# Kernel tuning notes

Hardware: AMD Instinct MI355X
Metric: run time of the kernel (lower is better)

The kernel has to match this reference:

```python
import jax, jax.numpy as jnp
import numpy as np

C = 256
RED = 2
CR = C // RED
B, D, H, W = 1, 16, 32, 32


def setup_inputs() -> dict:
    key = jax.random.key(0)
    ks = jax.random.split(key, 9)
    def w(k, o, i):
        return jax.random.normal(k, (o, i), dtype=jnp.float32) * (2.0 / i) ** 0.5
    return {
        "x": jax.random.normal(ks[0], (B, C, D, H, W), dtype=jnp.float32),
        "Wq": w(ks[1], CR, C), "bq": jnp.zeros((CR,), jnp.float32),
        "Wk": w(ks[2], CR, C), "bk": jnp.zeros((CR,), jnp.float32),
        "Wv": w(ks[3], CR, C), "bv": jnp.zeros((CR,), jnp.float32),
        "Wo": w(ks[4], C, CR) * 0.02, "bo": jnp.zeros((C,), jnp.float32),
    }


def reference(x, Wq, bq, Wk, bk, Wv, bv, Wo, bo):
    b, c, d, h, w = x.shape
    n = d * h * w
    scale = 1.0 / (c ** 0.5)
    xf = x.reshape(b, c, n)                      # [B, C, N]
    # 1x1x1 convs == per-voxel channel GEMMs
    q = jnp.einsum('oc,bcn->bno', Wq, xf) + bq   # [B, N, Cr]
    k = jnp.einsum('oc,bcn->bon', Wk, xf) + bk[:, None]  # [B, Cr, N]
    v = jnp.einsum('oc,bcn->bno', Wv, xf) + bv   # [B, N, Cr]
    attn = jnp.einsum('bnc,bcm->bnm', q, k) * scale      # [B, N, N]
    attn = jax.nn.softmax(attn, axis=-1)
    o = jnp.einsum('bnm,bmc->bnc', attn, v)      # [B, N, Cr]
    out = jnp.einsum('oc,bnc->bon', Wo, o) + bo[:, None]  # [B, C, N]
    return x + out.reshape(b, c, d, h, w)
```

## Files before the change

kernel.cpp:

```cpp
#include <hip/hip_runtime.h>

#define NTOK 16384
#define CCH  256
#define DH   128
#define KSPLIT 4

typedef float f32x4  __attribute__((ext_vector_type(4)));
typedef short bf16x8 __attribute__((ext_vector_type(8)));
typedef short bf16x4 __attribute__((ext_vector_type(4)));

__device__ __forceinline__ unsigned short f2bf(float f) {
    unsigned int u = __builtin_bit_cast(unsigned int, f);
    u += 0x7fffu + ((u >> 16) & 1u);
    return (unsigned short)(u >> 16);
}
__device__ __forceinline__ float bf2f(unsigned short h) {
    unsigned int u = ((unsigned int)h) << 16;
    return __builtin_bit_cast(float, u);
}
__device__ __forceinline__ unsigned short f2bf_fast(float f) {
    unsigned int u = __builtin_bit_cast(unsigned int, f);
    return (unsigned short)((u + 0x8000u) >> 16);
}
__device__ __forceinline__ void load_lds16(const unsigned short* g, unsigned short* l) {
    __builtin_amdgcn_global_load_lds(
        (const __attribute__((address_space(1))) unsigned int*)g,
        (__attribute__((address_space(3))) unsigned int*)l, 16, 0, 0);
}

__global__ __launch_bounds__(256) void prep_w(
    const float* __restrict__ Wq, const float* __restrict__ Wk,
    const float* __restrict__ Wv, const float* __restrict__ Wo,
    unsigned short* __restrict__ Wqkv_bf, unsigned short* __restrict__ Wo_bf)
{
    int idx4 = (blockIdx.x * 256 + threadIdx.x) * 4;
    if (idx4 < 98304) {
        int wch = idx4 >> 15;
        int off = idx4 & 32767;
        const float* W = (wch == 0) ? Wq : ((wch == 1) ? Wk : Wv);
        float4 v = *(const float4*)(W + off);
        bf16x4 pk = { (short)f2bf(v.x), (short)f2bf(v.y),
                      (short)f2bf(v.z), (short)f2bf(v.w) };
        *(bf16x4*)(Wqkv_bf + idx4) = pk;
    } else {
        int off = idx4 - 98304;
        float4 v = *(const float4*)(Wo + off);
        bf16x4 pk = { (short)f2bf(v.x), (short)f2bf(v.y),
                      (short)f2bf(v.z), (short)f2bf(v.w) };
        *(bf16x4*)(Wo_bf + off) = pk;
    }
}

__global__ __launch_bounds__(256) void qkv_fused(
    const float* __restrict__ x, const unsigned short* __restrict__ Wqkv_bf,
    const float* __restrict__ bq, const float* __restrict__ bk,
    const float* __restrict__ bv,
    unsigned short* __restrict__ Qb, unsigned short* __restrict__ Kb,
    unsigned short* __restrict__ Vb)
{
    __shared__ unsigned short lX[32 * 264];
    __shared__ unsigned short lW[3 * DH * 40];

    const int t    = threadIdx.x;
    const int wave = t >> 6, lane = t & 63, l16 = lane & 15, quad = lane >> 4;
    const int nt   = blockIdx.x;

#pragma unroll
    for (int pass = 0; pass < 8; ++pass) {
        int c  = pass * 32 + (t >> 3);
        int n4 = t & 7;
        float4 xv = *(const float4*)(x + c * NTOK + nt * 32 + n4 * 4);
        lX[(n4 * 4 + 0) * 264 + c] = f2bf(xv.x);
        lX[(n4 * 4 + 1) * 264 + c] = f2bf(xv.y);
        lX[(n4 * 4 + 2) * 264 + c] = f2bf(xv.z);
        lX[(n4 * 4 + 3) * 264 + c] = f2bf(xv.w);
    }

    f32x4 acc[3][2][2];
#pragma unroll
    for (int wch = 0; wch < 3; ++wch)
#pragma unroll
        for (int os = 0; os < 2; ++os)
#pragma unroll
            for (int ns = 0; ns < 2; ++ns) acc[wch][os][ns] = (f32x4){0, 0, 0, 0};

    for (int kc8 = 0; kc8 < 8; ++kc8) {
        __syncthreads();
#pragma unroll
        for (int wch = 0; wch < 3; ++wch) {
            const unsigned short* Wb = Wqkv_bf + wch * 32768;
#pragma unroll
            for (int p = 0; p < 2; ++p) {
                int s = p * 256 + t;
                int row = s >> 2, oct = s & 3;
                bf16x8 wv = *(const bf16x8*)(Wb + row * CCH + kc8 * 32 + oct * 8);
                *(bf16x8*)(&lW[wch * DH * 40 + row * 40 + oct * 8]) = wv;
            }
        }
        __syncthreads();

        bf16x8 bfr[2];
#pragma unroll
        for (int ns = 0; ns < 2; ++ns)
            bfr[ns] = *(const bf16x8*)(&lX[(ns * 16 + l16) * 264 + kc8 * 32 + quad * 8]);
#pragma unroll
        for (int wch = 0; wch < 3; ++wch)
#pragma unroll
            for (int os = 0; os < 2; ++os) {
                bf16x8 afr = *(const bf16x8*)(&lW[wch * DH * 40 + (wave * 32 + os * 16 + l16) * 40 + quad * 8]);
                acc[wch][os][0] = __builtin_amdgcn_mfma_f32_16x16x32_bf16(afr, bfr[0], acc[wch][os][0], 0, 0, 0);
                acc[wch][os][1] = __builtin_amdgcn_mfma_f32_16x16x32_bf16(afr, bfr[1], acc[wch][os][1], 0, 0, 0);
            }
    }

    unsigned short* lE = lX;

#pragma unroll
    for (int wch = 0; wch < 2; ++wch) {
        const float* bias = (wch == 0) ? bq : bk;
        const float oscale = (wch == 0) ? 0.0625f * 1.44269504f : 1.0f;
        __syncthreads();
#pragma unroll
        for (int os = 0; os < 2; ++os)
#pragma unroll
            for (int ns = 0; ns < 2; ++ns) {
                int o0 = wave * 32 + os * 16 + quad * 4;
                bf16x4 pk;
#pragma unroll
                for (int r = 0; r < 4; ++r)
                    pk[r] = (short)f2bf((acc[wch][os][ns][r] + bias[o0 + r]) * oscale);
                *(bf16x4*)(&lE[(ns * 16 + l16) * 136 + o0]) = pk;
            }
        __syncthreads();
        unsigned short* dst = (wch == 0) ? Qb : Kb;
#pragma unroll
        for (int it = 0; it < 2; ++it) {
            int idx = it * 256 + t;
            int n = idx >> 4, o8 = idx & 15;
            *(bf16x8*)(dst + (size_t)(nt * 32 + n) * DH + o8 * 8) =
                *(const bf16x8*)(&lE[n * 136 + o8 * 8]);
        }
    }

    __syncthreads();
#pragma unroll
    for (int os = 0; os < 2; ++os)
#pragma unroll
        for (int ns = 0; ns < 2; ++ns)
#pragma unroll
            for (int r = 0; r < 4; ++r) {
                int o = wave * 32 + os * 16 + quad * 4 + r;
                int n = ns * 16 + l16;
                lE[o * 40 + n] = f2bf(acc[2][os][ns][r] + bv[o]);
            }
    __syncthreads();
#pragma unroll
    for (int it = 0; it < 2; ++it) {
        int idx = it * 256 + t;
        int o = idx >> 2, f = idx & 3;
        *(bf16x8*)(Vb + (size_t)o * NTOK + nt * 32 + f * 8) =
            *(const bf16x8*)(&lE[o * 40 + f * 8]);
    }
}

#define LPS 64

__global__ __launch_bounds__(256, 2) void flash_attn(
    const unsigned short* __restrict__ Qb, const unsigned short* __restrict__ Kb,
    const unsigned short* __restrict__ Vb,
    unsigned short* __restrict__ P0, unsigned short* __restrict__ P123,
    float* __restrict__ lbuf, int niter)
{
    __shared__ unsigned short lK[64 * DH];
    __shared__ unsigned short lV[DH * 64];
    __shared__ unsigned short lP[4 * 32 * LPS];

    const int t    = threadIdx.x;
    const int wave = t >> 6, lane = t & 63, l16 = lane & 15, quad = lane >> 4;
    const int qrow0 = blockIdx.x * 128 + wave * 32;
    const int split = blockIdx.y;
    const int tile0 = split * niter;
    const int xorP  = (l16 & 7) << 3;

    bf16x8 qa[2][4];
#pragma unroll
    for (int h = 0; h < 2; ++h)
#pragma unroll
        for (int kc = 0; kc < 4; ++kc)
            qa[h][kc] = *(const bf16x8*)(Qb + (qrow0 + h * 16 + l16) * DH + kc * 32 + quad * 8);

    f32x4 acc[2][8];
#pragma unroll
    for (int h = 0; h < 2; ++h)
#pragma unroll
        for (int i = 0; i < 8; ++i) acc[h][i] = (f32x4){0, 0, 0, 0};
    float lpart[2] = {0.f, 0.f};

    for (int it = 0; it < niter; ++it) {
        __syncthreads();
        {
            const unsigned short* Kt = Kb + (size_t)(tile0 + it) * 64 * DH;
            const int vcol = (tile0 + it) * 64;
#pragma unroll
            for (int p = 0; p < 4; ++p) {
                int s = p * 256 + t;
                int key = s >> 4, c16 = s & 15;
                load_lds16(Kt + key * DH + ((c16 ^ (key & 15)) << 3),
                           &lK[(p * 256 + wave * 64) * 8]);
                int vr = s >> 3, vc = s & 7;
                load_lds16(Vb + vr * NTOK + vcol + ((vc ^ (vr & 7)) << 3),
                           &lV[(p * 256 + wave * 64) * 8]);
            }
        }
        __syncthreads();

        f32x4 sf[2][4];
#pragma unroll
        for (int h = 0; h < 2; ++h)
#pragma unroll
            for (int ns = 0; ns < 4; ++ns) sf[h][ns] = (f32x4){0, 0, 0, 0};
        __builtin_amdgcn_s_setprio(1);
#pragma unroll
        for (int kc = 0; kc < 4; ++kc) {
#pragma unroll
            for (int ns = 0; ns < 4; ++ns) {
                bf16x8 kb = *(const bf16x8*)(&lK[(ns * 16 + l16) * DH + (((kc * 4 + quad) ^ l16) << 3)]);
                sf[0][ns] = __builtin_amdgcn_mfma_f32_16x16x32_bf16(kb, qa[0][kc], sf[0][ns], 0, 0, 0);
                sf[1][ns] = __builtin_amdgcn_mfma_f32_16x16x32_bf16(kb, qa[1][kc], sf[1][ns], 0, 0, 0);
            }
        }
        __builtin_amdgcn_s_setprio(0);

        unsigned short* pb = &lP[wave * 32 * LPS];
#pragma unroll
        for (int h = 0; h < 2; ++h)
#pragma unroll
            for (int ns = 0; ns < 4; ++ns) {
                float p0 = __builtin_amdgcn_exp2f(sf[h][ns][0]);
                float p1 = __builtin_amdgcn_exp2f(sf[h][ns][1]);
                float p2 = __builtin_amdgcn_exp2f(sf[h][ns][2]);
                float p3 = __builtin_amdgcn_exp2f(sf[h][ns][3]);
                lpart[h] += (p0 + p1) + (p2 + p3);
                bf16x4 pk = { (short)f2bf_fast(p0), (short)f2bf_fast(p1),
                              (short)f2bf_fast(p2), (short)f2bf_fast(p3) };
                *(bf16x4*)(pb + (h * 16 + l16) * LPS + ((ns * 16 + quad * 4) ^ xorP)) = pk;
            }

        bf16x8 pa[2][2];
#pragma unroll
        for (int h = 0; h < 2; ++h)
#pragma unroll
            for (int half = 0; half < 2; ++half)
                pa[h][half] = *(const bf16x8*)(pb + (h * 16 + l16) * LPS + ((half * 32 + quad * 8) ^ xorP));

        __builtin_amdgcn_s_setprio(1);
#pragma unroll
        for (int ds = 0; ds < 8; ++ds) {
            bf16x8 vb0 = *(const bf16x8*)(&lV[(ds * 16 + l16) * 64 + ((quad ^ (l16 & 7)) << 3)]);
            bf16x8 vb1 = *(const bf16x8*)(&lV[(ds * 16 + l16) * 64 + (((4 + quad) ^ (l16 & 7)) << 3)]);
            acc[0][ds] = __builtin_amdgcn_mfma_f32_16x16x32_bf16(pa[0][0], vb0, acc[0][ds], 0, 0, 0);
            acc[0][ds] = __builtin_amdgcn_mfma_f32_16x16x32_bf16(pa[0][1], vb1, acc[0][ds], 0, 0, 0);
            acc[1][ds] = __builtin_amdgcn_mfma_f32_16x16x32_bf16(pa[1][0], vb0, acc[1][ds], 0, 0, 0);
            acc[1][ds] = __builtin_amdgcn_mfma_f32_16x16x32_bf16(pa[1][1], vb1, acc[1][ds], 0, 0, 0);
        }
        __builtin_amdgcn_s_setprio(0);
    }

    float lsum[2];
#pragma unroll
    for (int h = 0; h < 2; ++h) {
        float s = lpart[h];
        s += __shfl_xor(s, 16);
        s += __shfl_xor(s, 32);
        lsum[h] = s;
    }

    unsigned short* base = (split == 0) ? P0 : (P123 + (size_t)(split - 1) * NTOK * DH);
#pragma unroll
    for (int h = 0; h < 2; ++h) {
        float inv[4];
#pragma unroll
        for (int r = 0; r < 4; ++r)
            inv[r] = 1.0f / __shfl(lsum[h], quad * 4 + r, 16);
#pragma unroll
        for (int ds = 0; ds < 8; ++ds)
#pragma unroll
            for (int r = 0; r < 4; ++r) {
                int row = qrow0 + h * 16 + quad * 4 + r;
                base[row * DH + ds * 16 + l16] = f2bf(acc[h][ds][r] * inv[r]);
            }
        if (quad == 0)
            lbuf[split * NTOK + qrow0 + h * 16 + l16] = lsum[h];
    }
}

template <int NS>
__global__ __launch_bounds__(256) void combine(
    const unsigned short* __restrict__ P123, const float* __restrict__ lbuf,
    unsigned short* __restrict__ Ob)
{
    const int t = threadIdx.x;
    const int n  = blockIdx.x * 32 + (t >> 3);
    const int sg = t & 7;

    const unsigned short* Pp[NS];
    Pp[0] = Ob;
#pragma unroll
    for (int s = 1; s < NS; ++s) Pp[s] = P123 + (size_t)(s - 1) * NTOK * DH;

    float w[NS], den = 0.f;
#pragma unroll
    for (int s = 0; s < NS; ++s) { w[s] = lbuf[s * NTOK + n]; den += w[s]; }
    float invden = 1.0f / den;
#pragma unroll
    for (int s = 0; s < NS; ++s) w[s] *= invden;

#pragma unroll
    for (int j = 0; j < 2; ++j) {
        bf16x8 v[NS];
#pragma unroll
        for (int s = 0; s < NS; ++s)
            v[s] = *(const bf16x8*)(Pp[s] + n * DH + sg * 16 + j * 8);
        bf16x8 o;
#pragma unroll
        for (int e = 0; e < 8; ++e) {
            float a = 0.f;
#pragma unroll
            for (int s = 0; s < NS; ++s)
                a += w[s] * bf2f((unsigned short)v[s][e]);
            o[e] = (short)f2bf(a);
        }
        *(bf16x8*)(Ob + n * DH + sg * 16 + j * 8) = o;
    }
}

__global__ __launch_bounds__(256) void out_proj(
    const unsigned short* __restrict__ Wo_bf, const float* __restrict__ bo,
    const float* __restrict__ x, const unsigned short* __restrict__ Ob,
    float* __restrict__ out)
{
    __shared__ unsigned short lW[DH * 72];
    __shared__ float lsO[DH * 68];

    const int t    = threadIdx.x;
    const int wave = t >> 6, lane = t & 63, l16 = lane & 15, quad = lane >> 4;
    const int ch = blockIdx.x & 1;
    const int n0 = (blockIdx.x >> 1) * 64;
    const int c0 = ch * 128;

#pragma unroll
    for (int i = 0; i < 8; ++i) {
        int s = i * 256 + t;
        int row = s >> 4, oct = s & 15;
        bf16x8 wv = *(const bf16x8*)(Wo_bf + (c0 + row) * DH + oct * 8);
        *(bf16x8*)(&lW[row * 72 + oct * 8]) = wv;
    }
    __syncthreads();

    f32x4 acc[8];
#pragma unroll
    for (int i = 0; i < 8; ++i) acc[i] = (f32x4){0, 0, 0, 0};

#pragma unroll
    for (int kc = 0; kc < 4; ++kc) {
        bf16x8 bfr = *(const bf16x8*)(Ob + (n0 + wave * 16 + l16) * DH + kc * 32 + quad * 8);
#pragma unroll
        for (int cs = 0; cs < 8; ++cs) {
            bf16x8 afr = *(const bf16x8*)(&lW[(cs * 16 + l16) * 72 + kc * 32 + quad * 8]);
            acc[cs] = __builtin_amdgcn_mfma_f32_16x16x32_bf16(afr, bfr, acc[cs], 0, 0, 0);
        }
    }

#pragma unroll
    for (int cs = 0; cs < 8; ++cs)
#pragma unroll
        for (int r = 0; r < 4; ++r)
            lsO[(cs * 16 + quad * 4 + r) * 68 + wave * 16 + l16] = acc[cs][r];
    __syncthreads();

#pragma unroll
    for (int it = 0; it < 8; ++it) {
        int idx = it * 256 + t;
        int c  = idx >> 4;
        int n4 = idx & 15;
        float4 v = *(const float4*)(&lsO[c * 68 + n4 * 4]);
        float4 xv = *(const float4*)(x + (size_t)(c0 + c) * NTOK + n0 + n4 * 4);
        float b = bo[c0 + c];
        float4 o = { v.x + b + xv.x, v.y + b + xv.y, v.z + b + xv.z, v.w + b + xv.w };
        *(float4*)(out + (size_t)(c0 + c) * NTOK + n0 + n4 * 4) = o;
    }
}

template <int NS>
__global__ __launch_bounds__(256) void out_proj_fused(
    const unsigned short* __restrict__ Wo_bf, const float* __restrict__ bo,
    const float* __restrict__ x,
    const unsigned short* __restrict__ P0, const unsigned short* __restrict__ P123,
    const float* __restrict__ lbuf,
    float* __restrict__ out)
{
    __shared__ unsigned short lW[DH * 72];
    __shared__ float lsO[DH * 68];

    const int t    = threadIdx.x;
    const int wave = t >> 6, lane = t & 63, l16 = lane & 15, quad = lane >> 4;
    const int ch = blockIdx.x & 1;
    const int n0 = (blockIdx.x >> 1) * 64;
    const int c0 = ch * 128;

#pragma unroll
    for (int i = 0; i < 8; ++i) {
        int s = i * 256 + t;
        int row = s >> 4, oct = s & 15;
        bf16x8 wv = *(const bf16x8*)(Wo_bf + (c0 + row) * DH + oct * 8);
        *(bf16x8*)(&lW[row * 72 + oct * 8]) = wv;
    }

    const int n = n0 + wave * 16 + l16;
    const unsigned short* Pp[NS];
    Pp[0] = P0;
#pragma unroll
    for (int s = 1; s < NS; ++s) Pp[s] = P123 + (size_t)(s - 1) * NTOK * DH;
    float wgt[NS], den = 0.f;
#pragma unroll
    for (int s = 0; s < NS; ++s) { wgt[s] = lbuf[s * NTOK + n]; den += wgt[s]; }
    float invden = 1.0f / den;
#pragma unroll
    for (int s = 0; s < NS; ++s) wgt[s] *= invden;

    __syncthreads();

    f32x4 acc[8];
#pragma unroll
    for (int i = 0; i < 8; ++i) acc[i] = (f32x4){0, 0, 0, 0};

#pragma unroll
    for (int kc = 0; kc < 4; ++kc) {
        bf16x8 v[NS];
#pragma unroll
        for (int s = 0; s < NS; ++s)
            v[s] = *(const bf16x8*)(Pp[s] + (size_t)n * DH + kc * 32 + quad * 8);
        bf16x8 bfr;
#pragma unroll
        for (int e = 0; e < 8; ++e) {
            float a = 0.f;
#pragma unroll
            for (int s = 0; s < NS; ++s)
                a += wgt[s] * bf2f((unsigned short)v[s][e]);
            bfr[e] = (short)f2bf(a);
        }
#pragma unroll
        for (int cs = 0; cs < 8; ++cs) {
            bf16x8 afr = *(const bf16x8*)(&lW[(cs * 16 + l16) * 72 + kc * 32 + quad * 8]);
            acc[cs] = __builtin_amdgcn_mfma_f32_16x16x32_bf16(afr, bfr, acc[cs], 0, 0, 0);
        }
    }

#pragma unroll
    for (int cs = 0; cs < 8; ++cs)
#pragma unroll
        for (int r = 0; r < 4; ++r)
            lsO[(cs * 16 + quad * 4 + r) * 68 + wave * 16 + l16] = acc[cs][r];
    __syncthreads();

#pragma unroll
    for (int it = 0; it < 8; ++it) {
        int idx = it * 256 + t;
        int c  = idx >> 4;
        int n4 = idx & 15;
        float4 v = *(const float4*)(&lsO[c * 68 + n4 * 4]);
        float4 xv = *(const float4*)(x + (size_t)(c0 + c) * NTOK + n0 + n4 * 4);
        float b = bo[c0 + c];
        float4 o = { v.x + b + xv.x, v.y + b + xv.y, v.z + b + xv.z, v.w + b + xv.w };
        *(float4*)(out + (size_t)(c0 + c) * NTOK + n0 + n4 * 4) = o;
    }
}

extern "C" void kernel_launch(void* const* d_in, const int* in_sizes, int n_in,
                              void* d_out, int out_size, void* d_ws, size_t ws_size,
                              hipStream_t stream) {
    const float* x  = (const float*)d_in[0];
    const float* Wq = (const float*)d_in[1];
    const float* bq = (const float*)d_in[2];
    const float* Wk = (const float*)d_in[3];
    const float* bk = (const float*)d_in[4];
    const float* Wv = (const float*)d_in[5];
    const float* bv = (const float*)d_in[6];
    const float* Wo = (const float*)d_in[7];
    const float* bo = (const float*)d_in[8];
    float* out = (float*)d_out;

    char* w = (char*)d_ws;
    unsigned short* Qb = (unsigned short*)(w);
    unsigned short* Kb = (unsigned short*)(w + (4u << 20));
    unsigned short* Vb = (unsigned short*)(w + (8u << 20));
    unsigned short* Ob = (unsigned short*)(w + (12u << 20));

    const size_t lbuf_off  = (28u << 20);
    const size_t wbf_offA  = lbuf_off + KSPLIT * NTOK * sizeof(float);
    const size_t needA     = wbf_offA + (256u << 10);

    if (ws_size >= needA) {
        unsigned short* P123    = (unsigned short*)(w + (16u << 20));
        float*          lbuf    = (float*)(w + lbuf_off);
        unsigned short* Wqkv_bf = (unsigned short*)(w + wbf_offA);
        unsigned short* Wo_bf   = Wqkv_bf + 3 * DH * CCH;

        prep_w<<<128, 256, 0, stream>>>(Wq, Wk, Wv, Wo, Wqkv_bf, Wo_bf);
        qkv_fused<<<512, 256, 0, stream>>>(x, Wqkv_bf, bq, bk, bv, Qb, Kb, Vb);
        flash_attn<<<dim3(128, KSPLIT), 256, 0, stream>>>(Qb, Kb, Vb, Ob, P123, lbuf, 64);
        out_proj_fused<KSPLIT><<<512, 256, 0, stream>>>(Wo_bf, bo, x, Ob, P123, lbuf, out);
    } else {
        unsigned short* P123    = (unsigned short*)d_out;
        float*          lbuf    = (float*)((char*)d_out + (12u << 20));
        unsigned short* Wqkv_bf = (unsigned short*)(w + (16u << 20));
        unsigned short* Wo_bf   = Wqkv_bf + 3 * DH * CCH;

        prep_w<<<128, 256, 0, stream>>>(Wq, Wk, Wv, Wo, Wqkv_bf, Wo_bf);
        qkv_fused<<<512, 256, 0, stream>>>(x, Wqkv_bf, bq, bk, bv, Qb, Kb, Vb);
        flash_attn<<<dim3(128, 4), 256, 0, stream>>>(Qb, Kb, Vb, Ob, P123, lbuf, 64);
        combine<4><<<512, 256, 0, stream>>>(P123, lbuf, Ob);
        out_proj<<<512, 256, 0, stream>>>(Wo_bf, bo, x, Ob, out);
    }
}
```

Measured before the change: 233.6 us.

## Keep softmax probabilities in registers and permute V reads to match MFMA layout

```diff
diff --git a/kernel.cpp b/kernel.cpp
--- a/kernel.cpp
+++ b/kernel.cpp
@@ -163,8 +163,6 @@
     }
 }
 
-#define LPS 64
-
 __global__ __launch_bounds__(256, 2) void flash_attn(
     const unsigned short* __restrict__ Qb, const unsigned short* __restrict__ Kb,
     const unsigned short* __restrict__ Vb,
@@ -173,14 +171,12 @@
 {
     __shared__ unsigned short lK[64 * DH];
     __shared__ unsigned short lV[DH * 64];
-    __shared__ unsigned short lP[4 * 32 * LPS];
 
     const int t    = threadIdx.x;
     const int wave = t >> 6, lane = t & 63, l16 = lane & 15, quad = lane >> 4;
     const int qrow0 = blockIdx.x * 128 + wave * 32;
     const int split = blockIdx.y;
     const int tile0 = split * niter;
-    const int xorP  = (l16 & 7) << 3;
 
     bf16x8 qa[2][4];
 #pragma unroll
@@ -195,6 +191,9 @@
 #pragma unroll
         for (int i = 0; i < 8; ++i) acc[h][i] = (f32x4){0, 0, 0, 0};
     float lpart[2] = {0.f, 0.f};
+
+    const int vsub = (quad & 1) << 2;
+    const int qh   = quad >> 1;
 
     for (int it = 0; it < niter; ++it) {
         __syncthreads();
@@ -231,7 +230,7 @@
         }
         __builtin_amdgcn_s_setprio(0);
 
-        unsigned short* pb = &lP[wave * 32 * LPS];
+        bf16x8 pa[2][2];
 #pragma unroll
         for (int h = 0; h < 2; ++h)
 #pragma unroll
@@ -241,27 +240,25 @@
                 float p2 = __builtin_amdgcn_exp2f(sf[h][ns][2]);
                 float p3 = __builtin_amdgcn_exp2f(sf[h][ns][3]);
                 lpart[h] += (p0 + p1) + (p2 + p3);
-                bf16x4 pk = { (short)f2bf_fast(p0), (short)f2bf_fast(p1),
-                              (short)f2bf_fast(p2), (short)f2bf_fast(p3) };
-                *(bf16x4*)(pb + (h * 16 + l16) * LPS + ((ns * 16 + quad * 4) ^ xorP)) = pk;
-            }
-
-        bf16x8 pa[2][2];
-#pragma unroll
-        for (int h = 0; h < 2; ++h)
-#pragma unroll
-            for (int half = 0; half < 2; ++half)
-                pa[h][half] = *(const bf16x8*)(pb + (h * 16 + l16) * LPS + ((half * 32 + quad * 8) ^ xorP));
+                int hf = ns >> 1, e0 = (ns & 1) * 4;
+                pa[h][hf][e0 + 0] = (short)f2bf_fast(p0);
+                pa[h][hf][e0 + 1] = (short)f2bf_fast(p1);
+                pa[h][hf][e0 + 2] = (short)f2bf_fast(p2);
+                pa[h][hf][e0 + 3] = (short)f2bf_fast(p3);
+            }
 
         __builtin_amdgcn_s_setprio(1);
 #pragma unroll
         for (int ds = 0; ds < 8; ++ds) {
-            bf16x8 vb0 = *(const bf16x8*)(&lV[(ds * 16 + l16) * 64 + ((quad ^ (l16 & 7)) << 3)]);
-            bf16x8 vb1 = *(const bf16x8*)(&lV[(ds * 16 + l16) * 64 + (((4 + quad) ^ (l16 & 7)) << 3)]);
-            acc[0][ds] = __builtin_amdgcn_mfma_f32_16x16x32_bf16(pa[0][0], vb0, acc[0][ds], 0, 0, 0);
-            acc[0][ds] = __builtin_amdgcn_mfma_f32_16x16x32_bf16(pa[0][1], vb1, acc[0][ds], 0, 0, 0);
-            acc[1][ds] = __builtin_amdgcn_mfma_f32_16x16x32_bf16(pa[1][0], vb0, acc[1][ds], 0, 0, 0);
-            acc[1][ds] = __builtin_amdgcn_mfma_f32_16x16x32_bf16(pa[1][1], vb1, acc[1][ds], 0, 0, 0);
+            const unsigned short* vrow = &lV[(ds * 16 + l16) * 64];
+#pragma unroll
+            for (int hf = 0; hf < 2; ++hf) {
+                bf16x4 lo = *(const bf16x4*)(vrow + (((hf * 4 + qh) ^ (l16 & 7)) << 3) + vsub);
+                bf16x4 hi = *(const bf16x4*)(vrow + (((hf * 4 + 2 + qh) ^ (l16 & 7)) << 3) + vsub);
+                bf16x8 vb = { lo[0], lo[1], lo[2], lo[3], hi[0], hi[1], hi[2], hi[3] };
+                acc[0][ds] = __builtin_amdgcn_mfma_f32_16x16x32_bf16(pa[0][hf], vb, acc[0][ds], 0, 0, 0);
+                acc[1][ds] = __builtin_amdgcn_mfma_f32_16x16x32_bf16(pa[1][hf], vb, acc[1][ds], 0, 0, 0);
+            }
         }
         __builtin_amdgcn_s_setprio(0);
     }
```

Measured after the change: 246.0 us. 1.05x slower.
